# Kernel tuning notes

Measured on AMD Instinct MI355X. Metric: run time of the kernel, lower is better.

The kernel has to match this reference:

```python
import jax, jax.numpy as jnp
import numpy as np

NORM_SCALE = float(np.sqrt(1.0 / (128 * 4 * 4)))  # from module __init__
TEMP = 30.0
NORM_EPS = 1e-5


def setup_inputs() -> dict:
    key = jax.random.key(0)
    k1, k2, k3, k4, k5, k6 = jax.random.split(key, 6)
    b, n, c, h, w = 16, 4, 128, 32, 32
    return {
        "f_list1": jax.random.normal(k1, (b, n, c, h, w), dtype=jnp.float32),
        "f_list2": jax.random.normal(k2, (b, n, c, h, w), dtype=jnp.float32),
        "t_pos1": jax.random.normal(k3, (1, 1, c), dtype=jnp.float32),
        "t_pos2": jax.random.normal(k4, (1, 1, c), dtype=jnp.float32),
        "W_qk_w": jax.random.normal(k5, (32, c), dtype=jnp.float32) * (1.0 / np.sqrt(c)),
        "W_qk_b": jax.random.normal(k6, (32,), dtype=jnp.float32) * 0.01,
    }


def _l2_normalize(x, eps=1e-12):
    # torch F.normalize(p=2, dim=-1): x / max(||x||, eps)
    nrm = jnp.sqrt(jnp.sum(x * x, axis=-1, keepdims=True))
    return x / jnp.maximum(nrm, eps)


def reference(f_list1, f_list2, t_pos1, t_pos2, W_qk_w, W_qk_b):
    b, n, c, h, w = f_list1.shape
    hw = h * w
    # (b*n, hw, c) token-major layout + learned positional offsets
    f_l1 = f_list1.reshape(b * n, c, hw).transpose(0, 2, 1) + t_pos1
    f_l2 = f_list2.reshape(b * n, c, hw).transpose(0, 2, 1) + t_pos2
    # shared QK projection to head dim 32
    f_q = _l2_normalize(jnp.einsum('bsc,dc->bsd', f_l1, W_qk_w) + W_qk_b)
    f_k = _l2_normalize(jnp.einsum('bsc,dc->bsd', f_l2, W_qk_w) + W_qk_b)
    # cosine-similarity attention with fixed temperature 30
    attn = jax.nn.softmax(TEMP * jnp.einsum('bqd,bkd->bqk', f_q, f_k), axis=-1)
    f_r = jnp.einsum('bqk,bkc->bqc', attn, f_l2) + f_l2  # value = f_l2, plus residual
    f_r = f_r.transpose(0, 2, 1).reshape(b * n, c, h, w)
    # InstanceL2Norm (size_average=True): x * scale * sqrt(C*H*W / (sum(x^2) + eps)) per sample
    ssq = jnp.sum(f_r * f_r, axis=(1, 2, 3), keepdims=True)
    return f_r * (NORM_SCALE * jnp.sqrt((c * h * w) / (ssq + NORM_EPS)))
```

## Files before the change

kernel.cpp:

```cpp
#include <hip/hip_runtime.h>
#include <math.h>

typedef short s16x8 __attribute__((ext_vector_type(8)));
typedef float f32x4 __attribute__((ext_vector_type(4)));
typedef __bf16 bf16_t;
typedef bf16_t bf16x4 __attribute__((ext_vector_type(4)));

#define MFMA16 __builtin_amdgcn_mfma_f32_16x16x32_bf16
#define C_DIM 128
#define S_DIM 1024

__global__ __launch_bounds__(256) void k_wt(const float* __restrict__ Ww,
                                            float* __restrict__ Wt) {
    for (int e = threadIdx.x; e < 32 * C_DIM; e += 256) {
        int d = e >> 7, c = e & (C_DIM - 1);
        Wt[c * 32 + d] = Ww[e];
    }
}

__global__ __launch_bounds__(256) void k_proj(
    const float* __restrict__ f1, const float* __restrict__ f2,
    const float* __restrict__ pos1, const float* __restrict__ pos2,
    const float* __restrict__ Wt, const float* __restrict__ Wb,
    bf16_t* __restrict__ fqb, bf16_t* __restrict__ fkb,
    bf16_t* __restrict__ Vtb) {
    __shared__ float LX1[16][260];
    __shared__ float LX2[16][260];
    const int tid = threadIdx.x;
    const int b = blockIdx.x >> 2;
    const int t0 = (blockIdx.x & 3) * 256;

    float q[32], k[32];
#pragma unroll
    for (int d = 0; d < 32; ++d) { q[d] = 0.f; k[d] = 0.f; }

    for (int cc = 0; cc < C_DIM; cc += 16) {
        __syncthreads();
#pragma unroll
        for (int it = 0; it < 4; ++it) {
            const int e4 = it * 256 + tid;
            const int r = e4 >> 6, t4 = (e4 & 63) << 2;
            const int c = cc + r;
            const size_t base = ((size_t)b * C_DIM + c) * S_DIM + t0 + t4;
            const float p1 = pos1[c], p2 = pos2[c];
            float4 v1 = *(const float4*)(f1 + base);
            float4 v2 = *(const float4*)(f2 + base);
            v1.x += p1; v1.y += p1; v1.z += p1; v1.w += p1;
            v2.x += p2; v2.y += p2; v2.z += p2; v2.w += p2;
            *(float4*)&LX1[r][t4] = v1;
            *(float4*)&LX2[r][t4] = v2;
            bf16x4 vb = {(bf16_t)v2.x, (bf16_t)v2.y, (bf16_t)v2.z, (bf16_t)v2.w};
            *(bf16x4*)(Vtb + base) = vb;
        }
        __syncthreads();
#pragma unroll 4
        for (int r = 0; r < 16; ++r) {
            const float a1 = LX1[r][tid];
            const float a2 = LX2[r][tid];
            const float* wrow = Wt + (cc + r) * 32;
#pragma unroll
            for (int d = 0; d < 32; ++d) {
                const float wv = wrow[d];
                q[d] = fmaf(wv, a1, q[d]);
                k[d] = fmaf(wv, a2, k[d]);
            }
        }
    }

    float sq = 0.f, sk = 0.f;
#pragma unroll
    for (int d = 0; d < 32; ++d) {
        q[d] += Wb[d]; k[d] += Wb[d];
        sq = fmaf(q[d], q[d], sq);
        sk = fmaf(k[d], k[d], sk);
    }
    const float rq = 30.0f / fmaxf(sqrtf(sq), 1e-12f);
    const float rk = 1.0f / fmaxf(sqrtf(sk), 1e-12f);
    const size_t g = (size_t)b * S_DIM + t0 + tid;
    bf16_t* oq = fqb + g * 32;
    bf16_t* ok = fkb + g * 32;
#pragma unroll
    for (int c4 = 0; c4 < 8; ++c4) {
        bf16x4 vq = {(bf16_t)(q[c4 * 4] * rq), (bf16_t)(q[c4 * 4 + 1] * rq),
                     (bf16_t)(q[c4 * 4 + 2] * rq), (bf16_t)(q[c4 * 4 + 3] * rq)};
        bf16x4 vk = {(bf16_t)(k[c4 * 4] * rk), (bf16_t)(k[c4 * 4 + 1] * rk),
                     (bf16_t)(k[c4 * 4 + 2] * rk), (bf16_t)(k[c4 * 4 + 3] * rk)};
        *(bf16x4*)(oq + c4 * 4) = vq;
        *(bf16x4*)(ok + c4 * 4) = vk;
    }
}

static __device__ __forceinline__ unsigned int pkbf(float a, float b) {
    union { bf16_t h[2]; unsigned int u; } z;
    z.h[0] = (bf16_t)a; z.h[1] = (bf16_t)b;
    return z.u;
}

__global__ __launch_bounds__(256) void k_attn(
    const bf16_t* __restrict__ fqb, const bf16_t* __restrict__ fkb,
    const bf16_t* __restrict__ Vtb, float* __restrict__ fr,
    float* __restrict__ ssq) {
    __shared__ __align__(16) bf16_t Ks[64][40];
    __shared__ __align__(16) bf16_t Vs[128][72];
    __shared__ float wred[4];

    const int tid = threadIdx.x;
    const int w = tid >> 6;
    const int lane = tid & 63;
    const int l15 = lane & 15;
    const int Q = lane >> 4;
    const int b = blockIdx.y;
    const int qw = blockIdx.x * 64 + w * 16;

    const s16x8 qa =
        *(const s16x8*)(fqb + ((size_t)b * S_DIM + qw + l15) * 32 + Q * 8);

    f32x4 acc[8];
    const f32x4 fz = {0.f, 0.f, 0.f, 0.f};
#pragma unroll
    for (int cg = 0; cg < 8; ++cg) acc[cg] = fz;
    float m = -1e30f, l = 0.f;
    const int srcbase = l15 + 32 * (Q & 1);
    const int nsel = Q >> 1;

    for (int kb = 0; kb < 16; ++kb) {
        const int k0 = kb * 64;
        __syncthreads();
        {
            const int row = tid >> 2, c8 = (tid & 3) * 8;
            *(s16x8*)&Ks[row][c8] =
                *(const s16x8*)(fkb + ((size_t)b * S_DIM + k0 + row) * 32 + c8);
        }
#pragma unroll
        for (int it = 0; it < 4; ++it) {
            const int e = it * 256 + tid;
            const int row = e >> 3, c8 = (e & 7) * 8;
            *(s16x8*)&Vs[row][c8] =
                *(const s16x8*)(Vtb + ((size_t)b * C_DIM + row) * S_DIM + k0 + c8);
        }
        __syncthreads();

        f32x4 sc[4];
#pragma unroll
        for (int n = 0; n < 4; ++n) {
            const s16x8 kf = *(const s16x8*)&Ks[l15 + 16 * n][Q * 8];
            sc[n] = MFMA16(kf, qa, fz, 0, 0, 0);
        }

        float mx = sc[0][0];
#pragma unroll
        for (int n = 0; n < 4; ++n)
#pragma unroll
            for (int s = 0; s < 4; ++s) mx = fmaxf(mx, sc[n][s]);
        mx = fmaxf(mx, __shfl_xor(mx, 16));
        mx = fmaxf(mx, __shfl_xor(mx, 32));

        if (!__all(mx <= m + 8.0f)) {
            const float mn = fmaxf(m, mx);
            const float corr = __expf(m - mn);
#pragma unroll
            for (int cg = 0; cg < 8; ++cg) {
                acc[cg][0] *= corr; acc[cg][1] *= corr;
                acc[cg][2] *= corr; acc[cg][3] *= corr;
            }
            l *= corr; m = mn;
        }

        float pv[4][4];
        float sum = 0.f;
#pragma unroll
        for (int n = 0; n < 4; ++n)
#pragma unroll
            for (int s = 0; s < 4; ++s) {
                pv[n][s] = __expf(sc[n][s] - m);
                sum += pv[n][s];
            }
        sum += __shfl_xor(sum, 16);
        sum += __shfl_xor(sum, 32);
        l += sum;

        unsigned int wpk[4][2];
#pragma unroll
        for (int n = 0; n < 4; ++n) {
            wpk[n][0] = pkbf(pv[n][0], pv[n][1]);
            wpk[n][1] = pkbf(pv[n][2], pv[n][3]);
        }

#pragma unroll
        for (int h = 0; h < 2; ++h) {
            union { unsigned int u[4]; s16x8 v; } pb;
#pragma unroll
            for (int half = 0; half < 2; ++half)
#pragma unroll
                for (int a = 0; a < 2; ++a) {
                    const int src = srcbase + 16 * half;
                    const unsigned int g0 = __shfl((int)wpk[2 * h][a], src);
                    const unsigned int g1 = __shfl((int)wpk[2 * h + 1][a], src);
                    pb.u[half * 2 + a] = nsel ? g1 : g0;
                }
#pragma unroll
            for (int cg = 0; cg < 8; ++cg) {
                const s16x8 va = *(const s16x8*)&Vs[16 * cg + l15][h * 32 + Q * 8];
                acc[cg] = MFMA16(va, pb.v, acc[cg], 0, 0, 0);
            }
        }
    }

    const float invq = 1.0f / l;

    float sp = 0.f;
#pragma unroll
    for (int cg = 0; cg < 8; ++cg) {
#pragma unroll
        for (int s = 0; s < 4; ++s) {
            const int c = 16 * cg + 4 * Q + s;
            const size_t idx = ((size_t)b * C_DIM + c) * S_DIM + qw + l15;
            const float val = acc[cg][s] * invq + (float)Vtb[idx];
            fr[idx] = val;
            sp = fmaf(val, val, sp);
        }
    }
    sp += __shfl_down(sp, 32);
    sp += __shfl_down(sp, 16);
    sp += __shfl_down(sp, 8);
    sp += __shfl_down(sp, 4);
    sp += __shfl_down(sp, 2);
    sp += __shfl_down(sp, 1);
    if (lane == 0) wred[w] = sp;
    __syncthreads();
    if (tid == 0)
        atomicAdd(&ssq[b], wred[0] + wred[1] + wred[2] + wred[3]);
}

__global__ __launch_bounds__(256) void k_out(float* __restrict__ fr,
                                             const float* __restrict__ ssq) {
    const int b = blockIdx.x >> 5;
    const float scale =
        0.022097086912079608f * sqrtf(131072.0f / (ssq[b] + 1e-5f));
    float4* p = (float4*)fr + (size_t)blockIdx.x * 1024;
#pragma unroll
    for (int it = 0; it < 4; ++it) {
        float4 v = p[it * 256 + threadIdx.x];
        v.x *= scale; v.y *= scale; v.z *= scale; v.w *= scale;
        p[it * 256 + threadIdx.x] = v;
    }
}

extern "C" void kernel_launch(void* const* d_in, const int* in_sizes, int n_in,
                              void* d_out, int out_size, void* d_ws,
                              size_t ws_size, hipStream_t stream) {
    const float* f1 = (const float*)d_in[0];
    const float* f2 = (const float*)d_in[1];
    const float* pos1 = (const float*)d_in[2];
    const float* pos2 = (const float*)d_in[3];
    const float* Ww = (const float*)d_in[4];
    const float* Wb = (const float*)d_in[5];
    float* out = (float*)d_out;

    bf16_t* fqb = (bf16_t*)d_ws;
    bf16_t* fkb = fqb + 2097152;
    bf16_t* Vtb = fkb + 2097152;
    float* Wt = (float*)((char*)d_ws + 25165824);
    float* ssq = (float*)((char*)d_ws + 25182208);

    k_wt<<<1, 256, 0, stream>>>(Ww, Wt);
    k_proj<<<256, 256, 0, stream>>>(f1, f2, pos1, pos2, Wt, Wb, fqb, fkb, Vtb);
    hipMemsetAsync(ssq, 0, 256, stream);
    k_attn<<<dim3(16, 64), 256, 0, stream>>>(fqb, fkb, Vtb, out, ssq);
    k_out<<<2048, 256, 0, stream>>>(out, ssq);
}
```

Before: 221.1 us.

## Restructure projection, split V conversion, fold log2e into exp2, XCD-aware attention grid

The projection kernel now splits the channel reduction across lane quarters, reduces the partials with cross-lane shuffles, and keeps the weights and positional offsets in shared memory. This removes the separate weight-transpose kernel and uses twice as many blocks. The bf16 value conversion moves into its own elementwise kernel, which reads f2 a second time from memory. The attention softmax uses exp2 with log2e folded into the query scale. The attention grid is remapped so that blocks of the same batch land on the same XCD, which should improve L2 reuse of K and V.

```diff
diff --git a/kernel.cpp b/kernel.cpp
--- a/kernel.cpp
+++ b/kernel.cpp
@@ -5,66 +5,76 @@
 typedef float f32x4 __attribute__((ext_vector_type(4)));
 typedef __bf16 bf16_t;
 typedef bf16_t bf16x4 __attribute__((ext_vector_type(4)));
+typedef bf16_t bf16x8 __attribute__((ext_vector_type(8)));
 
 #define MFMA16 __builtin_amdgcn_mfma_f32_16x16x32_bf16
 #define C_DIM 128
 #define S_DIM 1024
-
-__global__ __launch_bounds__(256) void k_wt(const float* __restrict__ Ww,
-                                            float* __restrict__ Wt) {
-    for (int e = threadIdx.x; e < 32 * C_DIM; e += 256) {
-        int d = e >> 7, c = e & (C_DIM - 1);
-        Wt[c * 32 + d] = Ww[e];
-    }
-}
-
-__global__ __launch_bounds__(256) void k_proj(
+#define LOG2E 1.44269504088896f
+
+__global__ __launch_bounds__(256) void k_v(const float* __restrict__ f2,
+                                           const float* __restrict__ pos2,
+                                           bf16_t* __restrict__ Vtb) {
+    const int i = blockIdx.x * 256 + threadIdx.x;
+    float4 v = ((const float4*)f2)[i];
+    const float p = pos2[(i >> 8) & (C_DIM - 1)];
+    bf16x4 o = {(bf16_t)(v.x + p), (bf16_t)(v.y + p),
+                (bf16_t)(v.z + p), (bf16_t)(v.w + p)};
+    *(bf16x4*)(Vtb + (size_t)i * 4) = o;
+}
+
+__global__ __launch_bounds__(512) void k_proj(
     const float* __restrict__ f1, const float* __restrict__ f2,
     const float* __restrict__ pos1, const float* __restrict__ pos2,
-    const float* __restrict__ Wt, const float* __restrict__ Wb,
-    bf16_t* __restrict__ fqb, bf16_t* __restrict__ fkb,
-    bf16_t* __restrict__ Vtb) {
-    __shared__ float LX1[16][260];
-    __shared__ float LX2[16][260];
+    const float* __restrict__ Ww, const float* __restrict__ Wb,
+    bf16_t* __restrict__ fqb, bf16_t* __restrict__ fkb) {
+    __shared__ float LW[32][4][36];
+    __shared__ float LP1[C_DIM], LP2[C_DIM];
     const int tid = threadIdx.x;
-    const int b = blockIdx.x >> 2;
-    const int t0 = (blockIdx.x & 3) * 256;
+    const int w = tid >> 6;
+    const int lane = tid & 63;
+    const int l15 = lane & 15;
+    const int Q = lane >> 4;
+    const int b = blockIdx.x >> 3;
+    const int t0 = (blockIdx.x & 7) * 128;
+
+#pragma unroll
+    for (int it = 0; it < 8; ++it) {
+        const int e = it * 512 + tid;
+        const int d = e >> 7, c = e & 127;
+        LW[c & 31][c >> 5][d] = Ww[e];
+    }
+    if (tid < C_DIM) { LP1[tid] = pos1[tid]; LP2[tid] = pos2[tid]; }
+    __syncthreads();
+
+    const int t = t0 + w * 16 + l15;
+    const float* x1 = f1 + (size_t)b * C_DIM * S_DIM + t;
+    const float* x2 = f2 + (size_t)b * C_DIM * S_DIM + t;
 
     float q[32], k[32];
 #pragma unroll
     for (int d = 0; d < 32; ++d) { q[d] = 0.f; k[d] = 0.f; }
 
-    for (int cc = 0; cc < C_DIM; cc += 16) {
-        __syncthreads();
-#pragma unroll
-        for (int it = 0; it < 4; ++it) {
-            const int e4 = it * 256 + tid;
-            const int r = e4 >> 6, t4 = (e4 & 63) << 2;
-            const int c = cc + r;
-            const size_t base = ((size_t)b * C_DIM + c) * S_DIM + t0 + t4;
-            const float p1 = pos1[c], p2 = pos2[c];
-            float4 v1 = *(const float4*)(f1 + base);
-            float4 v2 = *(const float4*)(f2 + base);
-            v1.x += p1; v1.y += p1; v1.z += p1; v1.w += p1;
-            v2.x += p2; v2.y += p2; v2.z += p2; v2.w += p2;
-            *(float4*)&LX1[r][t4] = v1;
-            *(float4*)&LX2[r][t4] = v2;
-            bf16x4 vb = {(bf16_t)v2.x, (bf16_t)v2.y, (bf16_t)v2.z, (bf16_t)v2.w};
-            *(bf16x4*)(Vtb + base) = vb;
-        }
-        __syncthreads();
 #pragma unroll 4
-        for (int r = 0; r < 16; ++r) {
-            const float a1 = LX1[r][tid];
-            const float a2 = LX2[r][tid];
-            const float* wrow = Wt + (cc + r) * 32;
-#pragma unroll
-            for (int d = 0; d < 32; ++d) {
-                const float wv = wrow[d];
-                q[d] = fmaf(wv, a1, q[d]);
-                k[d] = fmaf(wv, a2, k[d]);
-            }
-        }
+    for (int j = 0; j < 32; ++j) {
+        const int c = Q * 32 + j;
+        const float a1 = x1[(size_t)c * S_DIM] + LP1[c];
+        const float a2 = x2[(size_t)c * S_DIM] + LP2[c];
+        const float* wr = &LW[j][Q][0];
+#pragma unroll
+        for (int d = 0; d < 32; ++d) {
+            const float wv = wr[d];
+            q[d] = fmaf(wv, a1, q[d]);
+            k[d] = fmaf(wv, a2, k[d]);
+        }
+    }
+
+#pragma unroll
+    for (int d = 0; d < 32; ++d) {
+        q[d] += __shfl_xor(q[d], 16);
+        q[d] += __shfl_xor(q[d], 32);
+        k[d] += __shfl_xor(k[d], 16);
+        k[d] += __shfl_xor(k[d], 32);
     }
 
     float sq = 0.f, sk = 0.f;
@@ -74,20 +84,18 @@
         sq = fmaf(q[d], q[d], sq);
         sk = fmaf(k[d], k[d], sk);
     }
-    const float rq = 30.0f / fmaxf(sqrtf(sq), 1e-12f);
+    const float rq = (30.0f * LOG2E) / fmaxf(sqrtf(sq), 1e-12f);
     const float rk = 1.0f / fmaxf(sqrtf(sk), 1e-12f);
-    const size_t g = (size_t)b * S_DIM + t0 + tid;
-    bf16_t* oq = fqb + g * 32;
-    bf16_t* ok = fkb + g * 32;
-#pragma unroll
-    for (int c4 = 0; c4 < 8; ++c4) {
-        bf16x4 vq = {(bf16_t)(q[c4 * 4] * rq), (bf16_t)(q[c4 * 4 + 1] * rq),
-                     (bf16_t)(q[c4 * 4 + 2] * rq), (bf16_t)(q[c4 * 4 + 3] * rq)};
-        bf16x4 vk = {(bf16_t)(k[c4 * 4] * rk), (bf16_t)(k[c4 * 4 + 1] * rk),
-                     (bf16_t)(k[c4 * 4 + 2] * rk), (bf16_t)(k[c4 * 4 + 3] * rk)};
-        *(bf16x4*)(oq + c4 * 4) = vq;
-        *(bf16x4*)(ok + c4 * 4) = vk;
-    }
+
+    const size_t g = (size_t)b * S_DIM + t;
+    bf16x8 vq, vk;
+#pragma unroll
+    for (int jj = 0; jj < 8; ++jj) {
+        vq[jj] = (bf16_t)(q[Q * 8 + jj] * rq);
+        vk[jj] = (bf16_t)(k[Q * 8 + jj] * rk);
+    }
+    *(bf16x8*)(fqb + g * 32 + Q * 8) = vq;
+    *(bf16x8*)(fkb + g * 32 + Q * 8) = vk;
 }
 
 static __device__ __forceinline__ unsigned int pkbf(float a, float b) {
@@ -109,8 +117,13 @@
     const int lane = tid & 63;
     const int l15 = lane & 15;
     const int Q = lane >> 4;
-    const int b = blockIdx.y;
-    const int qw = blockIdx.x * 64 + w * 16;
+
+    const int ell = blockIdx.x;
+    const int xcd = ell & 7;
+    const int slot = ell >> 3;
+    const int b = (slot >> 4) * 8 + xcd;
+    const int qb = slot & 15;
+    const int qw = qb * 64 + w * 16;
 
     const s16x8 qa =
         *(const s16x8*)(fqb + ((size_t)b * S_DIM + qw + l15) * 32 + Q * 8);
@@ -155,9 +168,9 @@
         mx = fmaxf(mx, __shfl_xor(mx, 16));
         mx = fmaxf(mx, __shfl_xor(mx, 32));
 
-        if (!__all(mx <= m + 8.0f)) {
+        if (!__all(mx <= m + 11.5416f)) {
             const float mn = fmaxf(m, mx);
-            const float corr = __expf(m - mn);
+            const float corr = exp2f(m - mn);
 #pragma unroll
             for (int cg = 0; cg < 8; ++cg) {
                 acc[cg][0] *= corr; acc[cg][1] *= corr;
@@ -172,7 +185,7 @@
         for (int n = 0; n < 4; ++n)
 #pragma unroll
             for (int s = 0; s < 4; ++s) {
-                pv[n][s] = __expf(sc[n][s] - m);
+                pv[n][s] = exp2f(sc[n][s] - m);
                 sum += pv[n][s];
             }
         sum += __shfl_xor(sum, 16);
@@ -260,12 +273,11 @@
     bf16_t* fqb = (bf16_t*)d_ws;
     bf16_t* fkb = fqb + 2097152;
     bf16_t* Vtb = fkb + 2097152;
-    float* Wt = (float*)((char*)d_ws + 25165824);
-    float* ssq = (float*)((char*)d_ws + 25182208);
-
-    k_wt<<<1, 256, 0, stream>>>(Ww, Wt);
-    k_proj<<<256, 256, 0, stream>>>(f1, f2, pos1, pos2, Wt, Wb, fqb, fkb, Vtb);
+    float* ssq = (float*)((char*)d_ws + 25165824);
+
+    k_proj<<<512, 512, 0, stream>>>(f1, f2, pos1, pos2, Ww, Wb, fqb, fkb);
+    k_v<<<8192, 256, 0, stream>>>(f2, pos2, Vtb);
     hipMemsetAsync(ssq, 0, 256, stream);
-    k_attn<<<dim3(16, 64), 256, 0, stream>>>(fqb, fkb, Vtb, out, ssq);
+    k_attn<<<1024, 256, 0, stream>>>(fqb, fkb, Vtb, out, ssq);
     k_out<<<2048, 256, 0, stream>>>(out, ssq);
 }
```

After: 214.9 us. -2.8%, faster.
